# Performance work log

Measured on AMD Instinct MI355X. Metric: run time of the kernel, lower is better.

Reference implementation:

```python
import jax, jax.numpy as jnp
from jax import lax
import numpy as np

B, N, C, V, NS = 4, 20000, 256, 300, 1024  # batch, seeds, feat dim, views, fps samples
EPS = 1e-5  # BatchNorm eps (torch default)
GRASP_THRESH = 0.09


def bn(x, g, b, m, v):
    # inference-mode BatchNorm1d over channel dim of x: [B, C, N]
    return (x - m[:, None]) * (g[:, None] / jnp.sqrt(v[:, None] + EPS)) + b[:, None]


def conv1x1(x, w, b):
    # 1x1 Conv1d == channel matmul. x: [B, Cin, N], w: [Cout, Cin], b: [Cout]
    return jnp.einsum('oi,bin->bon', w, x) + b[None, :, None]


def fps_masked(xyz, mask):
    """Furthest point sampling restricted to mask==True points.
    Matches pointnet2 FPS run on the masked subset: start at the first valid
    point, then repeatedly pick argmax of min-distance-to-selected among valid
    points. Invalid points get distance -1 so they are never selected.
    xyz: [N,3], mask: [N] bool -> [NS] int indices into the full point set."""
    dists0 = jnp.where(mask, jnp.float32(1e10), jnp.float32(-1.0))
    first = jnp.argmax(mask)  # index of first valid point

    def step(carry, _):
        dists, last = carry
        d = jnp.sum((xyz - xyz[last]) ** 2, axis=-1)
        dists = jnp.minimum(dists, jnp.where(mask, d, jnp.float32(-1.0)))
        return (dists, jnp.argmax(dists)), last

    _, inds = lax.scan(step, (dists0, first), None, length=NS)
    return inds


def grasp_views(num_view):
    # graspnetAPI generate_grasp_views: fibonacci sphere sampling
    phi = (np.sqrt(5.0) - 1.0) / 2.0
    i = np.arange(num_view)
    z = (2 * i + 1) / num_view - 1
    r = np.sqrt(np.maximum(1 - z * z, 0.0))
    x = r * np.cos(2 * np.pi * i * phi)
    y = r * np.sin(2 * np.pi * i * phi)
    return jnp.asarray(np.stack([x, y, z], 1).astype(np.float32))  # [V,3]


def viewpoint_to_matrix(towards, angle):
    # graspnetAPI batch_viewpoint_params_to_matrix. towards: [M,3], angle: [M]
    zeros = jnp.zeros_like(angle)
    ones = jnp.ones_like(angle)
    axis_x = towards
    axis_y = jnp.stack([-axis_x[:, 1], axis_x[:, 0], zeros], -1)
    ny = jnp.linalg.norm(axis_y, axis=-1, keepdims=True)
    axis_y = jnp.where(ny == 0, jnp.asarray([0.0, 1.0, 0.0], towards.dtype), axis_y)
    axis_x = axis_x / jnp.linalg.norm(axis_x, axis=-1, keepdims=True)
    axis_y = axis_y / jnp.linalg.norm(axis_y, axis=-1, keepdims=True)
    axis_z = jnp.cross(axis_x, axis_y)
    sin, cos = jnp.sin(angle), jnp.cos(angle)
    R1 = jnp.stack([ones, zeros, zeros, zeros, cos, -sin, zeros, sin, cos], -1).reshape(-1, 3, 3)
    R2 = jnp.stack([axis_x, axis_y, axis_z], -1)
    return R2 @ R1


def setup_inputs() -> dict:
    key = jax.random.key(0)
    ks = jax.random.split(key, 8)

    def w(k, shape, s=0.05):
        return jax.random.normal(k, shape, jnp.float32) * s

    return dict(
        seed_xyz=jax.random.normal(ks[0], (B, N, 3), jnp.float32),
        seed_features=jax.random.normal(ks[1], (B, C, N), jnp.float32),
        # graspable_head: conv-bn-relu-conv
        gh_w1=w(ks[2], (C, C)), gh_b1=jnp.zeros(C), gh_g1=jnp.ones(C), gh_be1=jnp.zeros(C),
        gh_m1=jnp.zeros(C), gh_v1=jnp.ones(C),
        gh_w2=w(ks[3], (1, C)), gh_b2=jnp.zeros(1),
        # view scoring convs
        w1=w(ks[4], (C, C)), b1=jnp.zeros(C), g1=jnp.ones(C), be1=jnp.zeros(C), m1=jnp.zeros(C), v1=jnp.ones(C),
        w2=w(ks[5], (V, C)), b2=jnp.zeros(V), g2=jnp.ones(V), be2=jnp.zeros(V), m2=jnp.zeros(V), v2=jnp.ones(V),
        w3=w(ks[6], (V, V)), b3=jnp.zeros(V),
    )


def reference(seed_xyz, seed_features, gh_w1, gh_b1, gh_g1, gh_be1, gh_m1, gh_v1, gh_w2, gh_b2,
              w1, b1, g1, be1, m1, v1, w2, b2, g2, be2, m2, v2, w3, b3):
    # graspable head -> graspness score [B, N]
    x = jax.nn.relu(bn(conv1x1(seed_features, gh_w1, gh_b1), gh_g1, gh_be1, gh_m1, gh_v1))
    graspness_score = conv1x1(x, gh_w2, gh_b2)[:, 0]
    mask = graspness_score > GRASP_THRESH

    # per-batch masked FPS (vectorized over batch via vmap)
    graspable_inds = jax.vmap(fps_masked)(seed_xyz, mask)  # [B, NS] int

    graspable_xyz = jnp.take_along_axis(seed_xyz, graspable_inds[:, :, None], axis=1)  # [B,NS,3]
    graspable_features = jnp.take_along_axis(
        seed_features.transpose(0, 2, 1), graspable_inds[:, :, None], axis=1
    ).transpose(0, 2, 1)  # [B,C,NS]
    fp2_graspness = jnp.take_along_axis(graspness_score, graspable_inds, axis=1)  # [B,NS]

    f = jax.nn.relu(bn(conv1x1(graspable_features, w1, b1), g1, be1, m1, v1))
    f = jax.nn.relu(bn(conv1x1(f, w2, b2), g2, be2, m2, v2))
    f = conv1x1(f, w3, b3)
    view_score = f.transpose(0, 2, 1)  # [B, NS, V]

    top_view_scores = jnp.max(view_score, axis=2)
    top_view_inds = jnp.argmax(view_score, axis=2)  # [B, NS]

    template_views = grasp_views(V)  # [V, 3]
    vp_xyz = template_views[top_view_inds]  # [B, NS, 3]
    vp_rot = viewpoint_to_matrix(-vp_xyz.reshape(-1, 3),
                                 jnp.zeros(B * NS, jnp.float32)).reshape(B, NS, 3, 3)

    return (graspness_score, graspable_inds, graspable_xyz, graspable_features,
            fp2_graspness, view_score, top_view_inds, top_view_scores, vp_xyz, vp_rot)
```

## Files before the change

### kernel.cpp

```cpp
#include <hip/hip_runtime.h>
#include <math.h>

#define NB 4
#define NPTS 20000
#define NC 256
#define NV 300
#define NSAMP 1024

#define O_GS    0
#define O_INDS  80000
#define O_XYZ   84096
#define O_FEAT  96384
#define O_FP2   1144960
#define O_VS    1149056
#define O_TVI   2377856
#define O_TVS   2381952
#define O_VPX   2386048
#define O_ROT   2398336

#define FPS_T 512
#define MAXPP 40
#define LDSM  4096

__global__ __launch_bounds__(256, 1) void graspness_kernel(
    const float* __restrict__ feat, const float* __restrict__ w1,
    const float* __restrict__ b1, const float* __restrict__ g1,
    const float* __restrict__ be1, const float* __restrict__ m1,
    const float* __restrict__ v1, const float* __restrict__ w2,
    const float* __restrict__ b2, float* __restrict__ out)
{
    __shared__ float Fs[NC][64];
    __shared__ float Xs[NC][65];
    __shared__ float As[2][16][64];

    int b  = blockIdx.z;
    int n0 = blockIdx.x * 64;
    int tid = threadIdx.x;
    int tx = tid & 15, ty = tid >> 4;
    int rem = NPTS - n0; if (rem > 64) rem = 64;

    {
        int j  = tid & 63;
        int kb = tid >> 6;
        const float* fb = feat + (size_t)b * NC * NPTS + n0;
        bool ok = (j < rem);
#pragma unroll
        for (int r = 0; r < 64; ++r) {
            int k = r * 4 + kb;
            Fs[k][j] = ok ? fb[(size_t)k * NPTS + j] : 0.f;
        }
    }

#pragma unroll
    for (int p = 0; p < 4; ++p) {
        int m_l = ty + p * 16;
        As[0][tx][m_l] = w1[(size_t)m_l * NC + tx];
    }
    __syncthreads();

    float acc[4][4][4];

    for (int s = 0; s < 64; ++s) {
        int ob = s >> 4, kt = s & 15;

        if (kt == 0) {
#pragma unroll
            for (int i = 0; i < 4; ++i)
#pragma unroll
                for (int j = 0; j < 4; ++j)
#pragma unroll
                    for (int c = 0; c < 4; ++c) acc[i][j][c] = 0.f;
        }

        if (s + 1 < 64) {
            int ob2 = (s + 1) >> 4, kt2 = (s + 1) & 15;
#pragma unroll
            for (int p = 0; p < 4; ++p) {
                int m_l = ty + p * 16;
                As[(s + 1) & 1][tx][m_l] =
                    w1[(size_t)(ob2 * 64 + m_l) * NC + kt2 * 16 + tx];
            }
        }

        const int buf = s & 1;
#pragma unroll
        for (int kk = 0; kk < 16; ++kk) {
            float4 a = *reinterpret_cast<const float4*>(&As[buf][kk][ty * 4]);
            float4 f = *reinterpret_cast<const float4*>(&Fs[kt * 16 + kk][tx * 4]);
            const int c = kk & 3;
            acc[0][0][c] += a.x * f.x; acc[0][1][c] += a.x * f.y;
            acc[0][2][c] += a.x * f.z; acc[0][3][c] += a.x * f.w;
            acc[1][0][c] += a.y * f.x; acc[1][1][c] += a.y * f.y;
            acc[1][2][c] += a.y * f.z; acc[1][3][c] += a.y * f.w;
            acc[2][0][c] += a.z * f.x; acc[2][1][c] += a.z * f.y;
            acc[2][2][c] += a.z * f.z; acc[2][3][c] += a.z * f.w;
            acc[3][0][c] += a.w * f.x; acc[3][1][c] += a.w * f.y;
            acc[3][2][c] += a.w * f.z; acc[3][3][c] += a.w * f.w;
        }

        if (kt == 15) {
#pragma unroll
            for (int i = 0; i < 4; ++i) {
                int o = ob * 64 + ty * 4 + i;
                float bo = b1[o];
                float sc = g1[o] / sqrtf(v1[o] + 1e-5f);
                float mo = m1[o], beo = be1[o];
#pragma unroll
                for (int j = 0; j < 4; ++j) {
                    float y = (acc[i][j][0] + acc[i][j][1]) +
                              (acc[i][j][2] + acc[i][j][3]) + bo;
                    float r = (y - mo) * sc + beo;
                    r = fmaxf(r, 0.f);
                    Xs[o][tx * 4 + j] = r;
                }
            }
        }
        __syncthreads();
    }

    if (tid < 64 && tid < rem) {
        float gs = 0.f;
#pragma unroll 8
        for (int o = 0; o < NC; ++o) {
            gs += w2[o] * Xs[o][tid];
        }
        out[(size_t)b * NPTS + n0 + tid] = gs + b2[0];
    }
}

template<int CTRL>
__device__ __forceinline__ unsigned long long dpp_u64(unsigned long long x)
{
    int lo = __builtin_amdgcn_update_dpp(0, (int)(unsigned)(x & 0xffffffffull),
                                         CTRL, 0xF, 0xF, false);
    int hi = __builtin_amdgcn_update_dpp(0, (int)(unsigned)(x >> 32),
                                         CTRL, 0xF, 0xF, false);
    return ((unsigned long long)(unsigned)hi << 32) | (unsigned)lo;
}

template<int TIER, bool USE_LDS>
__device__ __forceinline__ void fps_core2(
    int t, int M, int cnt2,
    const float* __restrict__ cxg, const float* __restrict__ cyg,
    const float* __restrict__ czg,
    const float* __restrict__ cxL, const float* __restrict__ cyL,
    const float* __restrict__ czL,
    int* __restrict__ hist, unsigned long long (*pkL)[8])
{
    int mybase = t * cnt2;
    int mycount = M - mybase;
    if (mycount > cnt2) mycount = cnt2;
    if (mycount < 0) mycount = 0;

    float rx[TIER], ry[TIER], rz[TIER], dd[TIER];
#pragma unroll
    for (int j = 0; j < TIER; ++j) {
        if (j < mycount) {
            rx[j] = USE_LDS ? cxL[mybase + j] : cxg[mybase + j];
            ry[j] = USE_LDS ? cyL[mybase + j] : cyg[mybase + j];
            rz[j] = USE_LDS ? czL[mybase + j] : czg[mybase + j];
            dd[j] = 1e10f;
        }
    }

    float wx = USE_LDS ? cxL[0] : cxg[0];
    float wy = USE_LDS ? cyL[0] : cyg[0];
    float wz = USE_LDS ? czL[0] : czg[0];
    int winner = 0;
    int w = t >> 6;

    for (int it = 0; it < NSAMP; ++it) {
        if (t == 0) hist[it] = winner;

        float bv = -2.f; int bc = 0x7fffffff;
#pragma unroll
        for (int j = 0; j < TIER; ++j) {
            if (j < mycount) {
                float dx = __fsub_rn(rx[j], wx);
                float dy = __fsub_rn(ry[j], wy);
                float dz = __fsub_rn(rz[j], wz);
                float d  = __fadd_rn(__fadd_rn(__fmul_rn(dx, dx), __fmul_rn(dy, dy)),
                                     __fmul_rn(dz, dz));
                float nd = fminf(dd[j], d);
                dd[j] = nd;
                if (nd > bv) { bv = nd; bc = mybase + j; }
            }
        }

        unsigned long long pk = (bc == 0x7fffffff)
            ? 0ull
            : (((unsigned long long)__float_as_uint(bv) << 32) | (unsigned)(~bc));

        { unsigned long long o = dpp_u64<0xB1>(pk);  if (o > pk) pk = o; }
        { unsigned long long o = dpp_u64<0x4E>(pk);  if (o > pk) pk = o; }
        { unsigned long long o = dpp_u64<0x124>(pk); if (o > pk) pk = o; }
        { unsigned long long o = dpp_u64<0x128>(pk); if (o > pk) pk = o; }
        { unsigned long long o = dpp_u64<0x142>(pk); if (o > pk) pk = o; }
        { unsigned long long o = dpp_u64<0x143>(pk); if (o > pk) pk = o; }

        int par = it & 1;
        if ((t & 63) == 63) pkL[par][w] = pk;
        __syncthreads();

        unsigned long long a0 = pkL[par][0], a1 = pkL[par][1];
        unsigned long long a2 = pkL[par][2], a3 = pkL[par][3];
        unsigned long long a4 = pkL[par][4], a5 = pkL[par][5];
        unsigned long long a6 = pkL[par][6], a7 = pkL[par][7];
        if (a1 > a0) a0 = a1;
        if (a3 > a2) a2 = a3;
        if (a5 > a4) a4 = a5;
        if (a7 > a6) a6 = a7;
        if (a2 > a0) a0 = a2;
        if (a6 > a4) a4 = a6;
        if (a4 > a0) a0 = a4;

        int pos = (int)(~(unsigned)(a0 & 0xffffffffull));
        winner = pos;
        wx = USE_LDS ? cxL[pos] : cxg[pos];
        wy = USE_LDS ? cyL[pos] : cyg[pos];
        wz = USE_LDS ? czL[pos] : czg[pos];
    }
}

__global__ __launch_bounds__(FPS_T, 2) void fps_kernel(
    const float* __restrict__ xyz, const float* __restrict__ gs,
    float* __restrict__ out_f, int* __restrict__ out_i,
    int* __restrict__ cidx, float* __restrict__ cx,
    float* __restrict__ cy, float* __restrict__ cz)
{
    int b = blockIdx.x;
    int t = threadIdx.x;
    __shared__ int sA[FPS_T], sB[FPS_T];
    __shared__ unsigned long long pkL[2][8];
    __shared__ int hist[NSAMP];
    __shared__ float cxL[LDSM], cyL[LDSM], czL[LDSM];
    __shared__ int cidxL[LDSM];

    const float* gsb = gs + (size_t)b * NPTS;
    const float* xb  = xyz + (size_t)b * NPTS * 3;

    int base = t * MAXPP;
    unsigned long long vmask = 0ull;
    int cnt = 0;
#pragma unroll
    for (int j = 0; j < MAXPP; ++j) {
        int p = base + j;
        if (p < NPTS) {
            if (gsb[p] > 0.09f) { vmask |= (1ull << j); ++cnt; }
        }
    }
    sA[t] = cnt;
    __syncthreads();
    int* src = sA; int* dst = sB;
    for (int off = 1; off < FPS_T; off <<= 1) {
        int v = src[t];
        if (t >= off) v += src[t - off];
        dst[t] = v;
        __syncthreads();
        int* tmp = src; src = dst; dst = tmp;
    }
    int M = src[FPS_T - 1];
    int excl = src[t] - cnt;
    bool useLds = (M <= LDSM);

    {
        int pos = excl;
#pragma unroll
        for (int j = 0; j < MAXPP; ++j) {
            if (vmask & (1ull << j)) {
                int p = base + j;
                if (useLds) {
                    cidxL[pos] = p;
                    cxL[pos] = xb[p * 3 + 0];
                    cyL[pos] = xb[p * 3 + 1];
                    czL[pos] = xb[p * 3 + 2];
                } else {
                    int gp = b * NPTS + pos;
                    cidx[gp] = p;
                    cx[gp] = xb[p * 3 + 0];
                    cy[gp] = xb[p * 3 + 1];
                    cz[gp] = xb[p * 3 + 2];
                }
                ++pos;
            }
        }
    }
    __syncthreads();

    if (M > 0) {
        const float* cxg = cx + b * NPTS;
        const float* cyg = cy + b * NPTS;
        const float* czg = cz + b * NPTS;

        if (useLds) {
            fps_core2<8, true>(t, M, (M + FPS_T - 1) / FPS_T, cxg, cyg, czg,
                               cxL, cyL, czL, hist, pkL);
        } else {
            int cnt2 = (M + FPS_T - 1) / FPS_T;
            if (cnt2 <= 16)      fps_core2<16, false>(t, M, cnt2, cxg, cyg, czg, cxL, cyL, czL, hist, pkL);
            else if (cnt2 <= 24) fps_core2<24, false>(t, M, cnt2, cxg, cyg, czg, cxL, cyL, czL, hist, pkL);
            else                 fps_core2<40, false>(t, M, cnt2, cxg, cyg, czg, cxL, cyL, czL, hist, pkL);
        }

        __syncthreads();
        for (int s = t; s < NSAMP; s += FPS_T) {
            int hp = hist[s];
            int oi = useLds ? cidxL[hp] : cidx[b * NPTS + hp];
            out_f[b * NSAMP + s] = (float)oi;
            out_i[b * NSAMP + s] = oi;
        }
    } else {
        for (int s = t; s < NSAMP; s += FPS_T) {
            out_f[b * NSAMP + s] = 0.f;
            out_i[b * NSAMP + s] = 0;
        }
    }
}

__global__ void gather_xyz_kernel(const float* __restrict__ xyz,
                                  const int* __restrict__ inds,
                                  float* __restrict__ dout)
{
    int i = blockIdx.x * 256 + threadIdx.x;
    if (i >= NB * NSAMP) return;
    int b = i >> 10;
    int ind = inds[i];
    const float* p = xyz + ((size_t)b * NPTS + ind) * 3;
    dout[O_XYZ + (size_t)i * 3 + 0] = p[0];
    dout[O_XYZ + (size_t)i * 3 + 1] = p[1];
    dout[O_XYZ + (size_t)i * 3 + 2] = p[2];
    dout[O_FP2 + i] = dout[O_GS + (size_t)b * NPTS + ind];
}

__global__ void gather_feat_kernel(const float* __restrict__ feat,
                                   const int* __restrict__ inds,
                                   float* __restrict__ dout)
{
    int c = blockIdx.x, b = blockIdx.y, s = threadIdx.x;
    int ind = inds[b * NSAMP + s];
    dout[O_FEAT + ((size_t)b * NC + c) * NSAMP + s] =
        feat[((size_t)b * NC + c) * NPTS + ind];
}

template<int EPI>
__global__ __launch_bounds__(256) void gemm_epi_kernel(
    const float* __restrict__ A, const float* __restrict__ Bsrc,
    int M, int K, size_t bstride,
    const float* __restrict__ bias, const float* __restrict__ gg,
    const float* __restrict__ bb, const float* __restrict__ mm,
    const float* __restrict__ vv,
    float* __restrict__ Cdst, size_t cstride)
{
    __shared__ float As[16][68];
    __shared__ float Bs[16][68];
    int tid = threadIdx.x;
    int n0 = blockIdx.x * 64;
    int m0 = blockIdx.y * 64;
    int b  = blockIdx.z;
    const float* Bb = Bsrc + (size_t)b * bstride;
    int tx = tid & 15, ty = tid >> 4;
    float acc[4][4] = {};
    int nk = (K + 15) >> 4;
    for (int kt = 0; kt < nk; ++kt) {
        int k0 = kt * 16;
#pragma unroll
        for (int p = 0; p < 4; ++p) {
            int m_l = ty + p * 16;
            int gm = m0 + m_l, gk = k0 + tx;
            float va = (gm < M && gk < K) ? A[(size_t)gm * K + gk] : 0.f;
            As[tx][m_l] = va;
        }
#pragma unroll
        for (int p = 0; p < 4; ++p) {
            int k_l = (tid >> 6) + p * 4;
            int n_l = tid & 63;
            int gk = k0 + k_l;
            float vb = (gk < K) ? Bb[(size_t)gk * NSAMP + n0 + n_l] : 0.f;
            Bs[k_l][n_l] = vb;
        }
        __syncthreads();
#pragma unroll
        for (int kk = 0; kk < 16; ++kk) {
            float a0 = As[kk][ty * 4 + 0], a1 = As[kk][ty * 4 + 1];
            float a2 = As[kk][ty * 4 + 2], a3 = As[kk][ty * 4 + 3];
            float c0 = Bs[kk][tx * 4 + 0], c1 = Bs[kk][tx * 4 + 1];
            float c2 = Bs[kk][tx * 4 + 2], c3 = Bs[kk][tx * 4 + 3];
            acc[0][0] += a0 * c0; acc[0][1] += a0 * c1; acc[0][2] += a0 * c2; acc[0][3] += a0 * c3;
            acc[1][0] += a1 * c0; acc[1][1] += a1 * c1; acc[1][2] += a1 * c2; acc[1][3] += a1 * c3;
            acc[2][0] += a2 * c0; acc[2][1] += a2 * c1; acc[2][2] += a2 * c2; acc[2][3] += a2 * c3;
            acc[3][0] += a3 * c0; acc[3][1] += a3 * c1; acc[3][2] += a3 * c2; acc[3][3] += a3 * c3;
        }
        __syncthreads();
    }
#pragma unroll
    for (int i = 0; i < 4; ++i) {
        int c = m0 + ty * 4 + i;
        if (c >= M) continue;
        float bi = bias[c];
        float scl = 0.f, sh = 0.f, mc = 0.f;
        if constexpr (EPI < 2) {
            scl = gg[c] / sqrtf(vv[c] + 1e-5f);
            sh = bb[c];
            mc = mm[c];
        }
#pragma unroll
        for (int j = 0; j < 4; ++j) {
            int n = n0 + tx * 4 + j;
            float v = acc[i][j] + bi;
            if constexpr (EPI < 2) {
                v = (v - mc) * scl + sh;
                v = fmaxf(v, 0.f);
                Cdst[(size_t)b * cstride + (size_t)c * NSAMP + n] = v;
            } else {
                Cdst[((size_t)b * NSAMP + n) * NV + c] = v;
            }
        }
    }
}

__global__ void view_kernel(float* __restrict__ dout)
{
    int i = blockIdx.x * 256 + threadIdx.x;
    if (i >= NB * NSAMP) return;
    const float* vs = dout + O_VS + (size_t)i * NV;
    float best = vs[0]; int bi = 0;
    for (int v = 1; v < NV; ++v) {
        float x = vs[v];
        if (x > best) { best = x; bi = v; }
    }
    dout[O_TVS + i] = best;
    dout[O_TVI + i] = (float)bi;

    const double PHI = (sqrt(5.0) - 1.0) / 2.0;
    double z = (2.0 * (double)bi + 1.0) / 300.0 - 1.0;
    double rr = sqrt(fmax(1.0 - z * z, 0.0));
    double ang = (2.0 * 3.14159265358979323846 * (double)bi) * PHI;
    float vx = (float)(rr * cos(ang));
    float vy = (float)(rr * sin(ang));
    float vz = (float)z;
    dout[O_VPX + (size_t)i * 3 + 0] = vx;
    dout[O_VPX + (size_t)i * 3 + 1] = vy;
    dout[O_VPX + (size_t)i * 3 + 2] = vz;

    float tx = -vx, ty = -vy, tz = -vz;
    float ayx = -ty, ayy = tx, ayz = 0.f;
    float ny = sqrtf(ayx * ayx + ayy * ayy + ayz * ayz);
    if (ny == 0.f) { ayx = 0.f; ayy = 1.f; ayz = 0.f; }
    float nx = sqrtf(tx * tx + ty * ty + tz * tz);
    float axx = tx / nx, axy = ty / nx, axz = tz / nx;
    float ny2 = sqrtf(ayx * ayx + ayy * ayy + ayz * ayz);
    ayx /= ny2; ayy /= ny2; ayz /= ny2;
    float azx = axy * ayz - axz * ayy;
    float azy = axz * ayx - axx * ayz;
    float azz = axx * ayy - axy * ayx;
    float* R = dout + O_ROT + (size_t)i * 9;
    R[0] = axx; R[1] = ayx; R[2] = azx;
    R[3] = axy; R[4] = ayy; R[5] = azy;
    R[6] = axz; R[7] = ayz; R[8] = azz;
}

extern "C" void kernel_launch(void* const* d_in, const int* in_sizes, int n_in,
                              void* d_out, int out_size, void* d_ws, size_t ws_size,
                              hipStream_t stream)
{
    const float* seed_xyz  = (const float*)d_in[0];
    const float* seed_feat = (const float*)d_in[1];
    const float* gh_w1 = (const float*)d_in[2];
    const float* gh_b1 = (const float*)d_in[3];
    const float* gh_g1 = (const float*)d_in[4];
    const float* gh_be1 = (const float*)d_in[5];
    const float* gh_m1 = (const float*)d_in[6];
    const float* gh_v1 = (const float*)d_in[7];
    const float* gh_w2 = (const float*)d_in[8];
    const float* gh_b2 = (const float*)d_in[9];
    const float* w1 = (const float*)d_in[10];
    const float* b1 = (const float*)d_in[11];
    const float* g1 = (const float*)d_in[12];
    const float* be1 = (const float*)d_in[13];
    const float* m1 = (const float*)d_in[14];
    const float* v1 = (const float*)d_in[15];
    const float* w2 = (const float*)d_in[16];
    const float* b2 = (const float*)d_in[17];
    const float* g2 = (const float*)d_in[18];
    const float* be2 = (const float*)d_in[19];
    const float* m2 = (const float*)d_in[20];
    const float* v2 = (const float*)d_in[21];
    const float* w3 = (const float*)d_in[22];
    const float* b3 = (const float*)d_in[23];

    float* out = (float*)d_out;

    int*   ws_inds = (int*)d_ws;
    int*   ws_cidx = ws_inds + NB * NSAMP;
    float* ws_cx = (float*)(ws_cidx + NB * NPTS);
    float* ws_cy = ws_cx + NB * NPTS;
    float* ws_cz = ws_cy + NB * NPTS;
    float* ws_g1 = ws_cz + NB * NPTS;
    float* ws_g2 = ws_g1 + (size_t)NB * NC * NSAMP;

    graspness_kernel<<<dim3(313, 1, NB), 256, 0, stream>>>(
        seed_feat, gh_w1, gh_b1, gh_g1, gh_be1, gh_m1, gh_v1, gh_w2, gh_b2,
        out + O_GS);

    fps_kernel<<<NB, FPS_T, 0, stream>>>(
        seed_xyz, out + O_GS, out + O_INDS, ws_inds,
        ws_cidx, ws_cx, ws_cy, ws_cz);

    gather_xyz_kernel<<<(NB * NSAMP + 255) / 256, 256, 0, stream>>>(
        seed_xyz, ws_inds, out);

    gather_feat_kernel<<<dim3(NC, NB), 1024, 0, stream>>>(
        seed_feat, ws_inds, out);

    gemm_epi_kernel<0><<<dim3(16, 4, NB), 256, 0, stream>>>(
        w1, out + O_FEAT, NC, NC, (size_t)NC * NSAMP,
        b1, g1, be1, m1, v1, ws_g1, (size_t)NC * NSAMP);

    gemm_epi_kernel<1><<<dim3(16, 5, NB), 256, 0, stream>>>(
        w2, ws_g1, NV, NC, (size_t)NC * NSAMP,
        b2, g2, be2, m2, v2, ws_g2, (size_t)NV * NSAMP);

    gemm_epi_kernel<2><<<dim3(16, 5, NB), 256, 0, stream>>>(
        w3, ws_g2, NV, NV, (size_t)NV * NSAMP,
        b3, nullptr, nullptr, nullptr, nullptr, out + O_VS, 0);

    view_kernel<<<(NB * NSAMP + 255) / 256, 256, 0, stream>>>(out);
}
```

Measured before the change: 1.324 ms.

## Double graspness kernel threads and stage view-score stores through LDS

The graspness MLP kernel now runs with 512 threads per block. Each thread computes a 2x4 output tile instead of 4x4, which cuts per-thread registers and spreads the load and compute over more waves. The weight-tile LDS buffer is padded to avoid bank conflicts. The final view-score GEMM now stages its 64x64 tile in shared memory, so the transposed [B,NS,V] stores are written row-contiguously instead of strided. The price is an extra LDS buffer and a barrier in that GEMM, and the large LDS footprint of the graspness kernel may still keep one block per CU.

```diff
diff --git a/kernel.cpp b/kernel.cpp
--- a/kernel.cpp
+++ b/kernel.cpp
@@ -22,7 +22,7 @@
 #define MAXPP 40
 #define LDSM  4096
 
-__global__ __launch_bounds__(256, 1) void graspness_kernel(
+__global__ __launch_bounds__(512, 2) void graspness_kernel(
     const float* __restrict__ feat, const float* __restrict__ w1,
     const float* __restrict__ b1, const float* __restrict__ g1,
     const float* __restrict__ be1, const float* __restrict__ m1,
@@ -31,12 +31,13 @@
 {
     __shared__ float Fs[NC][64];
     __shared__ float Xs[NC][65];
-    __shared__ float As[2][16][64];
+    __shared__ float As[2][16][66];
 
     int b  = blockIdx.z;
     int n0 = blockIdx.x * 64;
     int tid = threadIdx.x;
-    int tx = tid & 15, ty = tid >> 4;
+    int tx = tid & 15;
+    int ty = tid >> 4;
     int rem = NPTS - n0; if (rem > 64) rem = 64;
 
     {
@@ -45,27 +46,28 @@
         const float* fb = feat + (size_t)b * NC * NPTS + n0;
         bool ok = (j < rem);
 #pragma unroll
-        for (int r = 0; r < 64; ++r) {
-            int k = r * 4 + kb;
+        for (int r = 0; r < 32; ++r) {
+            int k = r * 8 + kb;
             Fs[k][j] = ok ? fb[(size_t)k * NPTS + j] : 0.f;
         }
     }
 
-#pragma unroll
-    for (int p = 0; p < 4; ++p) {
-        int m_l = ty + p * 16;
-        As[0][tx][m_l] = w1[(size_t)m_l * NC + tx];
+    {
+        int k_l = tid & 15;
+        int o_l = tid >> 4;
+        As[0][k_l][o_l]      = w1[(size_t)o_l * NC + k_l];
+        As[0][k_l][o_l + 32] = w1[(size_t)(o_l + 32) * NC + k_l];
     }
     __syncthreads();
 
-    float acc[4][4][4];
+    float acc[2][4][4];
 
     for (int s = 0; s < 64; ++s) {
         int ob = s >> 4, kt = s & 15;
 
         if (kt == 0) {
 #pragma unroll
-            for (int i = 0; i < 4; ++i)
+            for (int i = 0; i < 2; ++i)
 #pragma unroll
                 for (int j = 0; j < 4; ++j)
 #pragma unroll
@@ -74,34 +76,30 @@
 
         if (s + 1 < 64) {
             int ob2 = (s + 1) >> 4, kt2 = (s + 1) & 15;
-#pragma unroll
-            for (int p = 0; p < 4; ++p) {
-                int m_l = ty + p * 16;
-                As[(s + 1) & 1][tx][m_l] =
-                    w1[(size_t)(ob2 * 64 + m_l) * NC + kt2 * 16 + tx];
-            }
+            int k_l = tid & 15;
+            int o_l = tid >> 4;
+            As[(s + 1) & 1][k_l][o_l] =
+                w1[(size_t)(ob2 * 64 + o_l) * NC + kt2 * 16 + k_l];
+            As[(s + 1) & 1][k_l][o_l + 32] =
+                w1[(size_t)(ob2 * 64 + o_l + 32) * NC + kt2 * 16 + k_l];
         }
 
         const int buf = s & 1;
 #pragma unroll
         for (int kk = 0; kk < 16; ++kk) {
-            float4 a = *reinterpret_cast<const float4*>(&As[buf][kk][ty * 4]);
+            float2 a = *reinterpret_cast<const float2*>(&As[buf][kk][ty * 2]);
             float4 f = *reinterpret_cast<const float4*>(&Fs[kt * 16 + kk][tx * 4]);
             const int c = kk & 3;
             acc[0][0][c] += a.x * f.x; acc[0][1][c] += a.x * f.y;
             acc[0][2][c] += a.x * f.z; acc[0][3][c] += a.x * f.w;
             acc[1][0][c] += a.y * f.x; acc[1][1][c] += a.y * f.y;
             acc[1][2][c] += a.y * f.z; acc[1][3][c] += a.y * f.w;
-            acc[2][0][c] += a.z * f.x; acc[2][1][c] += a.z * f.y;
-            acc[2][2][c] += a.z * f.z; acc[2][3][c] += a.z * f.w;
-            acc[3][0][c] += a.w * f.x; acc[3][1][c] += a.w * f.y;
-            acc[3][2][c] += a.w * f.z; acc[3][3][c] += a.w * f.w;
         }
 
         if (kt == 15) {
 #pragma unroll
-            for (int i = 0; i < 4; ++i) {
-                int o = ob * 64 + ty * 4 + i;
+            for (int i = 0; i < 2; ++i) {
+                int o = ob * 64 + ty * 2 + i;
                 float bo = b1[o];
                 float sc = g1[o] / sqrtf(v1[o] + 1e-5f);
                 float mo = m1[o], beo = be1[o];
@@ -353,6 +351,7 @@
 {
     __shared__ float As[16][68];
     __shared__ float Bs[16][68];
+    __shared__ float Cs[64][65];
     int tid = threadIdx.x;
     int n0 = blockIdx.x * 64;
     int m0 = blockIdx.y * 64;
@@ -412,8 +411,17 @@
                 v = fmaxf(v, 0.f);
                 Cdst[(size_t)b * cstride + (size_t)c * NSAMP + n] = v;
             } else {
-                Cdst[((size_t)b * NSAMP + n) * NV + c] = v;
+                Cs[ty * 4 + i][tx * 4 + j] = v;
             }
+        }
+    }
+    if constexpr (EPI == 2) {
+        __syncthreads();
+        for (int idx = tid; idx < 64 * 64; idx += 256) {
+            int n_l = idx >> 6, c_l = idx & 63;
+            int c = m0 + c_l;
+            if (c < M)
+                Cdst[((size_t)b * NSAMP + n0 + n_l) * NV + c] = Cs[c_l][n_l];
         }
     }
 }
@@ -498,7 +506,7 @@
     float* ws_g1 = ws_cz + NB * NPTS;
     float* ws_g2 = ws_g1 + (size_t)NB * NC * NSAMP;
 
-    graspness_kernel<<<dim3(313, 1, NB), 256, 0, stream>>>(
+    graspness_kernel<<<dim3(313, 1, NB), 512, 0, stream>>>(
         seed_feat, gh_w1, gh_b1, gh_g1, gh_be1, gh_m1, gh_v1, gh_w2, gh_b2,
         out + O_GS);
 
```

Measured after the change: 1.227 ms. 7.4% less time.
